# Kernel optimization log

Hardware: AMD Instinct MI355X
Metric: run time of the kernel (lower is better)

## Reference

```python
import jax, jax.numpy as jnp
import numpy as np
from functools import partial

STRIDE = 32
NUM_CLASSES = 20
CONF_THRESH = 0.01
NMS_THRESH = 0.5
H = W = 96
C = 512


def setup_inputs() -> dict:
    key = jax.random.key(0)
    ks = jax.random.split(key, 6)
    cls_feat = jax.random.normal(ks[0], (1, C, H, W), dtype=jnp.float32)
    reg_feat = jax.random.normal(ks[1], (1, C, H, W), dtype=jnp.float32)
    # small init scale so sigmoid/exp stay in a realistic range
    obj_w = jax.random.normal(ks[2], (1, C), dtype=jnp.float32) * 0.05
    cls_w = jax.random.normal(ks[3], (NUM_CLASSES, C), dtype=jnp.float32) * 0.05
    reg_w = jax.random.normal(ks[4], (4, C), dtype=jnp.float32) * 0.05
    obj_b = jnp.zeros((1,), jnp.float32)
    cls_b = jnp.zeros((NUM_CLASSES,), jnp.float32)
    reg_b = jnp.zeros((4,), jnp.float32)
    return {"cls_feat": cls_feat, "reg_feat": reg_feat,
            "obj_w": obj_w, "obj_b": obj_b,
            "cls_w": cls_w, "cls_b": cls_b,
            "reg_w": reg_w, "reg_b": reg_b}


def _decode_and_score(cls_feat, reg_feat, obj_w, obj_b, cls_w, cls_b, reg_w, reg_b):
    # 1x1 convs == per-pixel matmul; permute(0,2,3,1).flatten(1,2), take batch 0
    _, _, h, w = cls_feat.shape
    obj = jnp.einsum('bchw,oc->bhwo', cls_feat, obj_w)[0].reshape(h * w, 1) + obj_b
    cls = jnp.einsum('bchw,oc->bhwo', cls_feat, cls_w)[0].reshape(h * w, NUM_CLASSES) + cls_b
    reg = jnp.einsum('bchw,oc->bhwo', reg_feat, reg_w)[0].reshape(h * w, 4) + reg_b
    scores_all = jax.nn.sigmoid(obj) * jax.nn.sigmoid(cls)            # [N, 20]
    # decode_boxes: grid of (x, y) cell coords, stride 32
    gy, gx = jnp.meshgrid(jnp.arange(h), jnp.arange(w), indexing='ij')
    grid = jnp.stack([gx, gy], axis=-1).reshape(-1, 2).astype(jnp.float32)
    ctr = (jax.nn.sigmoid(reg[:, :2]) + grid) * STRIDE               # [N, 2]
    wh = jnp.exp(reg[:, 2:]) * STRIDE                                # [N, 2]
    bboxes = jnp.concatenate([ctr - 0.5 * wh, ctr + 0.5 * wh], axis=-1)  # x1y1x2y2
    return bboxes, scores_all


@jax.jit
def reference(cls_feat, reg_feat, obj_w, obj_b, cls_w, cls_b, reg_w, reg_b):
    bboxes, scores_all = _decode_and_score(
        cls_feat, reg_feat, obj_w, obj_b, cls_w, cls_b, reg_w, reg_b)
    n = bboxes.shape[0]
    labels = jnp.argmax(scores_all, axis=1)                          # [N]
    scores = jnp.max(scores_all, axis=1)                             # [N]
    valid = scores >= CONF_THRESH
    # sort by score descending (invalid boxes pushed last)
    order = jnp.argsort(-jnp.where(valid, scores, -jnp.inf))
    b = bboxes[order]
    lab_s = labels[order]
    valid_s = valid[order]
    x1, y1, x2, y2 = b[:, 0], b[:, 1], b[:, 2], b[:, 3]
    areas = (x2 - x1) * (y2 - y1)
    # pairwise IoU, matching the numpy nms (1e-10 clamp on w/h)
    iw = jnp.maximum(1e-10, jnp.minimum(x2[:, None], x2[None, :]) - jnp.maximum(x1[:, None], x1[None, :]))
    ih = jnp.maximum(1e-10, jnp.minimum(y2[:, None], y2[None, :]) - jnp.maximum(y1[:, None], y1[None, :]))
    inter = iw * ih
    iou = inter / (areas[:, None] + areas[None, :] - inter)
    same_cls = lab_s[:, None] == lab_s[None, :]
    supp = (iou > NMS_THRESH) & same_cls                             # [N, N] suppression graph
    idx = jnp.arange(n)
    # greedy per-class NMS in score order: box i is kept iff no earlier
    # kept box of the same class has IoU > thresh with it
    def body(i, keep):
        suppressed = jnp.any(keep & supp[:, i] & (idx < i))
        return keep.at[i].set(valid_s[i] & ~suppressed)
    keep_s = jax.lax.fori_loop(0, n, body, jnp.zeros(n, dtype=bool))
    keep = jnp.zeros(n, dtype=bool).at[order].set(keep_s)            # unsort
    return bboxes, scores, labels, keep


if __name__ == '__main__':
    out = reference(**setup_inputs())
    print([o.shape for o in out], int(out[3].sum()))
```

## Files before the change

kernel.cpp:

```cpp
#include <hip/hip_runtime.h>

#define HW 9216
#define WIDTH 96
#define NCLS 20
#define NOUT 25
#define CAP 1024
#define NW 16

__global__ __launch_bounds__(256) void decode_kernel(
    const float* __restrict__ cls_feat, const float* __restrict__ reg_feat,
    const float* __restrict__ obj_w, const float* __restrict__ obj_b,
    const float* __restrict__ cls_w, const float* __restrict__ cls_b,
    const float* __restrict__ reg_w, const float* __restrict__ reg_b,
    float* __restrict__ out, unsigned* __restrict__ cnt,
    unsigned long long* __restrict__ keys)
{
    __shared__ float lds[512 * 28];
    const int tid = threadIdx.x;

    for (int i = tid; i < 25 * 512; i += 256) {
        int o = i >> 9, c = i & 511;
        float v;
        if (o == 0)        v = obj_w[c];
        else if (o < 21)   v = cls_w[(o - 1) * 512 + c];
        else               v = reg_w[(o - 21) * 512 + c];
        lds[c * 28 + o] = v;
    }
    __syncthreads();

    const int posL  = tid & 31;
    const int chunk = tid >> 5;
    const int p     = blockIdx.x * 32 + posL;
    const int cb    = chunk * 64;

    float acc[NOUT];
#pragma unroll
    for (int o = 0; o < NOUT; ++o) acc[o] = 0.f;

    const float* cf = cls_feat + cb * HW + p;
    const float* rf = reg_feat + cb * HW + p;

#pragma unroll 4
    for (int k = 0; k < 64; ++k) {
        float f = cf[k * HW];
        float g = rf[k * HW];
        const float4* w = (const float4*)(lds + (cb + k) * 28);
        float4 w0 = w[0], w1 = w[1], w2 = w[2], w3 = w[3], w4v = w[4], w5 = w[5], w6 = w[6];
        acc[0]  += f * w0.x;  acc[1]  += f * w0.y;  acc[2]  += f * w0.z;  acc[3]  += f * w0.w;
        acc[4]  += f * w1.x;  acc[5]  += f * w1.y;  acc[6]  += f * w1.z;  acc[7]  += f * w1.w;
        acc[8]  += f * w2.x;  acc[9]  += f * w2.y;  acc[10] += f * w2.z;  acc[11] += f * w2.w;
        acc[12] += f * w3.x;  acc[13] += f * w3.y;  acc[14] += f * w3.z;  acc[15] += f * w3.w;
        acc[16] += f * w4v.x; acc[17] += f * w4v.y; acc[18] += f * w4v.z; acc[19] += f * w4v.w;
        acc[20] += f * w5.x;
        acc[21] += g * w5.y;  acc[22] += g * w5.z;  acc[23] += g * w5.w;  acc[24] += g * w6.x;
    }

    __syncthreads();
    float* part = lds;
#pragma unroll
    for (int o = 0; o < NOUT; ++o) part[(chunk * 32 + posL) * NOUT + o] = acc[o];
    __syncthreads();

    float* dots = lds + 8 * 32 * NOUT;
    for (int t = tid; t < 32 * NOUT; t += 256) {
        int pos = t / NOUT, o = t - pos * NOUT;
        float s = 0.f;
#pragma unroll
        for (int c2 = 0; c2 < 8; ++c2) s += part[(c2 * 32 + pos) * NOUT + o];
        dots[t] = s;
    }
    __syncthreads();

    if (tid < 32) {
        const int pos = tid;
        const int pp  = blockIdx.x * 32 + pos;
        const float* d = dots + pos * NOUT;

        float obj  = d[0] + obj_b[0];
        float best = d[1] + cls_b[0];
        int   bk   = 0;
#pragma unroll
        for (int k = 1; k < NCLS; ++k) {
            float v = d[1 + k] + cls_b[k];
            if (v > best) { best = v; bk = k; }
        }
        float sobj  = 1.f / (1.f + expf(-obj));
        float scls  = 1.f / (1.f + expf(-best));
        float score = sobj * scls;

        float r0 = d[21] + reg_b[0], r1 = d[22] + reg_b[1];
        float r2 = d[23] + reg_b[2], r3 = d[24] + reg_b[3];
        float gx = (float)(pp % WIDTH), gy = (float)(pp / WIDTH);
        float cx = (1.f / (1.f + expf(-r0)) + gx) * 32.f;
        float cy = (1.f / (1.f + expf(-r1)) + gy) * 32.f;
        float bw = expf(r2) * 32.f;
        float bh = expf(r3) * 32.f;
        float hx = 0.5f * bw, hy = 0.5f * bh;

        ((float4*)out)[pp] = make_float4(cx - hx, cy - hy, cx + hx, cy + hy);
        out[HW * 4 + pp] = score;
        out[HW * 5 + pp] = (float)bk;
        out[HW * 6 + pp] = 0.f;

        if (score >= 0.01f) {
            unsigned slot = atomicAdd(&cnt[bk], 1u);
            if (slot < CAP) {
                unsigned sb = __float_as_uint(score) ^ 0xffffffffu;
                keys[bk * CAP + slot] = ((unsigned long long)sb << 32) | (unsigned)pp;
            }
        }
    }
}

__global__ __launch_bounds__(512) void sort_kernel(
    const unsigned* __restrict__ cnt, unsigned long long* __restrict__ keys)
{
    __shared__ unsigned long long a[CAP];
    const int c = blockIdx.x, t = threadIdx.x;
    unsigned m = cnt[c]; if (m > CAP) m = CAP;

    for (int i = t; i < CAP; i += 512)
        a[i] = (i < (int)m) ? keys[c * CAP + i] : 0xFFFFFFFFFFFFFFFFull;
    __syncthreads();

    for (int k = 2; k <= CAP; k <<= 1) {
        for (int j = k >> 1; j > 0; j >>= 1) {
            int i = ((t & ~(j - 1)) << 1) | (t & (j - 1));
            int p = i | j;
            unsigned long long x = a[i], y = a[p];
            bool up = ((i & k) == 0);
            if ((x > y) == up) { a[i] = y; a[p] = x; }
            __syncthreads();
        }
    }
    for (int i = t; i < (int)m; i += 512) keys[c * CAP + i] = a[i];
}

__global__ __launch_bounds__(1024) void build_kernel(
    const unsigned* __restrict__ cnt, const unsigned long long* __restrict__ keys,
    const float* __restrict__ bboxes, unsigned long long* __restrict__ mask)
{
    __shared__ float4 box[CAP];
    const int c = blockIdx.x >> 4, tile = blockIdx.x & 15;
    const int tid = threadIdx.x, wave = tid >> 6, lane = tid & 63;
    int m = (int)cnt[c]; if (m > CAP) m = CAP;
    const int rbase = tile << 6;
    if (rbase >= m) return;

    if (tid < m) {
        unsigned idx = (unsigned)(keys[c * CAP + tid] & 0xffffffffu);
        box[tid] = ((const float4*)bboxes)[idx];
    } else {
        box[tid] = make_float4(0.f, 0.f, 0.f, 0.f);
    }
    __syncthreads();

    unsigned long long* mrow = mask + (size_t)c * CAP * NW;
#pragma unroll 4
    for (int j = 0; j < 64; ++j) {
        const int row = rbase + (wave << 2) + (j >> 4);
        const int w   = j & 15;
        const float4 bi = box[row];
        const float4 bj = box[(w << 6) + lane];
        const float ai = (bi.z - bi.x) * (bi.w - bi.y);
        const float aj = (bj.z - bj.x) * (bj.w - bj.y);
        float iw = fminf(bi.z, bj.z) - fmaxf(bi.x, bj.x);
        float ih = fminf(bi.w, bj.w) - fmaxf(bi.y, bj.y);
        iw = fmaxf(iw, 1e-10f);
        ih = fmaxf(ih, 1e-10f);
        const float inter = iw * ih;
        const float iou = inter / (ai + aj - inter);
        unsigned long long word =
            __ballot((row < m) && (((w << 6) + lane) < m) && (iou > 0.5f));
        if (lane == 0) mrow[row * NW + w] = word;
    }
}

__device__ __forceinline__ unsigned long long uread64(unsigned long long v, int srclane) {
    unsigned lo = __builtin_amdgcn_readlane((unsigned)v, srclane);
    unsigned hi = __builtin_amdgcn_readlane((unsigned)(v >> 32), srclane);
    return ((unsigned long long)hi << 32) | lo;
}

__device__ __forceinline__ unsigned long long shflxor64(unsigned long long v, int m) {
    unsigned lo = __shfl_xor((unsigned)v, m, 64);
    unsigned hi = __shfl_xor((unsigned)(v >> 32), m, 64);
    return ((unsigned long long)hi << 32) | lo;
}

__global__ __launch_bounds__(64) void sweep_kernel(
    const unsigned* __restrict__ cnt, const unsigned long long* __restrict__ keys,
    const unsigned long long* __restrict__ mask, float* __restrict__ keep)
{
    const int c = blockIdx.x, lane = threadIdx.x;
    int m = (int)cnt[c]; if (m > CAP) m = CAP;
    const int nw = (m + 63) >> 6;
    const unsigned long long* mrow = mask + (size_t)c * CAP * NW;

    const int wsel = lane & 15;
    const int rof  = lane >> 4;

    unsigned long long remw = 0;
    for (int w = 0; w < nw; ++w) {
        const int i0 = w << 6;
        const int nb = min(64, m - i0);

        unsigned long long mykey =
            (lane < nb) ? keys[c * CAP + i0 + lane] : 0ull;
        unsigned long long myrow =
            (lane < nb) ? mrow[(size_t)(i0 + lane) * NW + w] : 0ull;

        unsigned long long rw[16];
#pragma unroll
        for (int j = 0; j < 16; ++j) {
            const int r = i0 + rof + (j << 2);
            rw[j] = (r < m && wsel < nw)
                        ? mrow[(size_t)r * NW + wsel] : 0ull;
        }

        unsigned long long cur  = uread64(remw, w);
        unsigned long long kept = 0;
#pragma unroll
        for (int b = 0; b < 64; ++b) {
            unsigned long long v = uread64(myrow, b);
            unsigned long long alive = ((cur >> b) & 1ull) ^ 1ull;
            kept |= alive << b;
            cur |= v & (0ull - alive);
        }
        if (nb < 64) kept &= (1ull << nb) - 1ull;

        if (lane < nb && ((kept >> lane) & 1ull))
            keep[(unsigned)(mykey & 0xffffffffu)] = 1.0f;

        unsigned long long part = 0;
#pragma unroll
        for (int j = 0; j < 16; ++j) {
            const int b = rof + (j << 2);
            part |= rw[j] & (0ull - ((kept >> b) & 1ull));
        }
        part |= shflxor64(part, 16);
        part |= shflxor64(part, 32);
        if (lane < NW) remw |= part;
    }
}

extern "C" void kernel_launch(void* const* d_in, const int* in_sizes, int n_in,
                              void* d_out, int out_size, void* d_ws, size_t ws_size,
                              hipStream_t stream)
{
    const float* cls_feat = (const float*)d_in[0];
    const float* reg_feat = (const float*)d_in[1];
    const float* obj_w    = (const float*)d_in[2];
    const float* obj_b    = (const float*)d_in[3];
    const float* cls_w    = (const float*)d_in[4];
    const float* cls_b    = (const float*)d_in[5];
    const float* reg_w    = (const float*)d_in[6];
    const float* reg_b    = (const float*)d_in[7];

    float* out = (float*)d_out;
    unsigned* cnt = (unsigned*)d_ws;
    unsigned long long* keys = (unsigned long long*)((char*)d_ws + 256);
    unsigned long long* mask = (unsigned long long*)((char*)d_ws + 256 + NCLS * CAP * 8);

    hipMemsetAsync(d_ws, 0, 256, stream);

    decode_kernel<<<288, 256, 0, stream>>>(cls_feat, reg_feat, obj_w, obj_b,
                                           cls_w, cls_b, reg_w, reg_b,
                                           out, cnt, keys);
    sort_kernel<<<NCLS, 512, 0, stream>>>(cnt, keys);
    build_kernel<<<NCLS * 16, 1024, 0, stream>>>(cnt, keys, out, mask);
    sweep_kernel<<<NCLS, 64, 0, stream>>>(cnt, keys, mask, out + HW * 6);
}
```

Measured before the change: 187.5 us.

## Split GEMM into channel-parallel stage, fuse sort, mask build and sweep into one kernel

The 1x1-conv GEMM now runs as a separate stage where each block handles 256 pixels for one 64-channel group, reading weights directly from global/scalar memory, and writes partial sums to workspace. A second kernel reduces the partials and decodes boxes. Sort, IoU mask construction and the greedy sweep are merged into a single per-class 1024-thread kernel that uses a register/shuffle bitonic sort and keeps the suppression mask in LDS. The memset is replaced by zeroing counters inside the first kernel. This removes launches and global mask traffic, at the cost of a partial-sum round trip and a serial per-class block with heavy LDS use.

```diff
diff --git a/kernel.cpp b/kernel.cpp
--- a/kernel.cpp
+++ b/kernel.cpp
@@ -7,240 +7,218 @@
 #define CAP 1024
 #define NW 16
 
-__global__ __launch_bounds__(256) void decode_kernel(
+#define WS_KEYS   256
+#define WS_PART   164096
+
+__global__ __launch_bounds__(256) void gemm_stage1(
     const float* __restrict__ cls_feat, const float* __restrict__ reg_feat,
-    const float* __restrict__ obj_w, const float* __restrict__ obj_b,
-    const float* __restrict__ cls_w, const float* __restrict__ cls_b,
-    const float* __restrict__ reg_w, const float* __restrict__ reg_b,
+    const float* __restrict__ obj_w, const float* __restrict__ cls_w,
+    const float* __restrict__ reg_w, float* __restrict__ partial,
+    unsigned* __restrict__ cnt)
+{
+    if (blockIdx.x == 0 && threadIdx.x < 64) cnt[threadIdx.x] = 0u;
+
+    const int g   = blockIdx.x & 7;
+    const int pos = (blockIdx.x >> 3) * 256 + threadIdx.x;
+    const int cb  = g * 64;
+
+    float acc[NOUT];
+#pragma unroll
+    for (int o = 0; o < NOUT; ++o) acc[o] = 0.f;
+
+    const float* cf = cls_feat + (size_t)cb * HW + pos;
+    const float* rf = reg_feat + (size_t)cb * HW + pos;
+
+#pragma unroll 16
+    for (int k = 0; k < 64; ++k) {
+        const int c = cb + k;
+        float f = cf[(size_t)k * HW];
+        float h = rf[(size_t)k * HW];
+        acc[0] += f * obj_w[c];
+#pragma unroll
+        for (int j = 0; j < 20; ++j) acc[1 + j] += f * cls_w[j * 512 + c];
+#pragma unroll
+        for (int j = 0; j < 4; ++j)  acc[21 + j] += h * reg_w[j * 512 + c];
+    }
+
+    float* pg = partial + (size_t)g * NOUT * HW + pos;
+#pragma unroll
+    for (int o = 0; o < NOUT; ++o) pg[(size_t)o * HW] = acc[o];
+}
+
+__global__ __launch_bounds__(256) void decode_stage2(
+    const float* __restrict__ partial,
+    const float* __restrict__ obj_b, const float* __restrict__ cls_b,
+    const float* __restrict__ reg_b,
     float* __restrict__ out, unsigned* __restrict__ cnt,
     unsigned long long* __restrict__ keys)
 {
-    __shared__ float lds[512 * 28];
-    const int tid = threadIdx.x;
-
-    for (int i = tid; i < 25 * 512; i += 256) {
-        int o = i >> 9, c = i & 511;
-        float v;
-        if (o == 0)        v = obj_w[c];
-        else if (o < 21)   v = cls_w[(o - 1) * 512 + c];
-        else               v = reg_w[(o - 21) * 512 + c];
-        lds[c * 28 + o] = v;
-    }
-    __syncthreads();
-
-    const int posL  = tid & 31;
-    const int chunk = tid >> 5;
-    const int p     = blockIdx.x * 32 + posL;
-    const int cb    = chunk * 64;
-
-    float acc[NOUT];
-#pragma unroll
-    for (int o = 0; o < NOUT; ++o) acc[o] = 0.f;
-
-    const float* cf = cls_feat + cb * HW + p;
-    const float* rf = reg_feat + cb * HW + p;
-
-#pragma unroll 4
-    for (int k = 0; k < 64; ++k) {
-        float f = cf[k * HW];
-        float g = rf[k * HW];
-        const float4* w = (const float4*)(lds + (cb + k) * 28);
-        float4 w0 = w[0], w1 = w[1], w2 = w[2], w3 = w[3], w4v = w[4], w5 = w[5], w6 = w[6];
-        acc[0]  += f * w0.x;  acc[1]  += f * w0.y;  acc[2]  += f * w0.z;  acc[3]  += f * w0.w;
-        acc[4]  += f * w1.x;  acc[5]  += f * w1.y;  acc[6]  += f * w1.z;  acc[7]  += f * w1.w;
-        acc[8]  += f * w2.x;  acc[9]  += f * w2.y;  acc[10] += f * w2.z;  acc[11] += f * w2.w;
-        acc[12] += f * w3.x;  acc[13] += f * w3.y;  acc[14] += f * w3.z;  acc[15] += f * w3.w;
-        acc[16] += f * w4v.x; acc[17] += f * w4v.y; acc[18] += f * w4v.z; acc[19] += f * w4v.w;
-        acc[20] += f * w5.x;
-        acc[21] += g * w5.y;  acc[22] += g * w5.z;  acc[23] += g * w5.w;  acc[24] += g * w6.x;
-    }
-
-    __syncthreads();
-    float* part = lds;
-#pragma unroll
-    for (int o = 0; o < NOUT; ++o) part[(chunk * 32 + posL) * NOUT + o] = acc[o];
-    __syncthreads();
-
-    float* dots = lds + 8 * 32 * NOUT;
-    for (int t = tid; t < 32 * NOUT; t += 256) {
-        int pos = t / NOUT, o = t - pos * NOUT;
+    const int pp = blockIdx.x * 256 + threadIdx.x;
+
+    float d[NOUT];
+#pragma unroll
+    for (int o = 0; o < NOUT; ++o) {
         float s = 0.f;
 #pragma unroll
-        for (int c2 = 0; c2 < 8; ++c2) s += part[(c2 * 32 + pos) * NOUT + o];
-        dots[t] = s;
-    }
-    __syncthreads();
-
-    if (tid < 32) {
-        const int pos = tid;
-        const int pp  = blockIdx.x * 32 + pos;
-        const float* d = dots + pos * NOUT;
-
-        float obj  = d[0] + obj_b[0];
-        float best = d[1] + cls_b[0];
-        int   bk   = 0;
-#pragma unroll
-        for (int k = 1; k < NCLS; ++k) {
-            float v = d[1 + k] + cls_b[k];
-            if (v > best) { best = v; bk = k; }
-        }
-        float sobj  = 1.f / (1.f + expf(-obj));
-        float scls  = 1.f / (1.f + expf(-best));
-        float score = sobj * scls;
-
-        float r0 = d[21] + reg_b[0], r1 = d[22] + reg_b[1];
-        float r2 = d[23] + reg_b[2], r3 = d[24] + reg_b[3];
-        float gx = (float)(pp % WIDTH), gy = (float)(pp / WIDTH);
-        float cx = (1.f / (1.f + expf(-r0)) + gx) * 32.f;
-        float cy = (1.f / (1.f + expf(-r1)) + gy) * 32.f;
-        float bw = expf(r2) * 32.f;
-        float bh = expf(r3) * 32.f;
-        float hx = 0.5f * bw, hy = 0.5f * bh;
-
-        ((float4*)out)[pp] = make_float4(cx - hx, cy - hy, cx + hx, cy + hy);
-        out[HW * 4 + pp] = score;
-        out[HW * 5 + pp] = (float)bk;
-        out[HW * 6 + pp] = 0.f;
-
-        if (score >= 0.01f) {
-            unsigned slot = atomicAdd(&cnt[bk], 1u);
-            if (slot < CAP) {
-                unsigned sb = __float_as_uint(score) ^ 0xffffffffu;
-                keys[bk * CAP + slot] = ((unsigned long long)sb << 32) | (unsigned)pp;
-            }
-        }
-    }
-}
-
-__global__ __launch_bounds__(512) void sort_kernel(
-    const unsigned* __restrict__ cnt, unsigned long long* __restrict__ keys)
-{
-    __shared__ unsigned long long a[CAP];
-    const int c = blockIdx.x, t = threadIdx.x;
-    unsigned m = cnt[c]; if (m > CAP) m = CAP;
-
-    for (int i = t; i < CAP; i += 512)
-        a[i] = (i < (int)m) ? keys[c * CAP + i] : 0xFFFFFFFFFFFFFFFFull;
-    __syncthreads();
-
-    for (int k = 2; k <= CAP; k <<= 1) {
-        for (int j = k >> 1; j > 0; j >>= 1) {
-            int i = ((t & ~(j - 1)) << 1) | (t & (j - 1));
-            int p = i | j;
-            unsigned long long x = a[i], y = a[p];
-            bool up = ((i & k) == 0);
-            if ((x > y) == up) { a[i] = y; a[p] = x; }
-            __syncthreads();
-        }
-    }
-    for (int i = t; i < (int)m; i += 512) keys[c * CAP + i] = a[i];
-}
-
-__global__ __launch_bounds__(1024) void build_kernel(
-    const unsigned* __restrict__ cnt, const unsigned long long* __restrict__ keys,
-    const float* __restrict__ bboxes, unsigned long long* __restrict__ mask)
-{
-    __shared__ float4 box[CAP];
-    const int c = blockIdx.x >> 4, tile = blockIdx.x & 15;
-    const int tid = threadIdx.x, wave = tid >> 6, lane = tid & 63;
-    int m = (int)cnt[c]; if (m > CAP) m = CAP;
-    const int rbase = tile << 6;
-    if (rbase >= m) return;
-
-    if (tid < m) {
-        unsigned idx = (unsigned)(keys[c * CAP + tid] & 0xffffffffu);
-        box[tid] = ((const float4*)bboxes)[idx];
-    } else {
-        box[tid] = make_float4(0.f, 0.f, 0.f, 0.f);
-    }
-    __syncthreads();
-
-    unsigned long long* mrow = mask + (size_t)c * CAP * NW;
-#pragma unroll 4
-    for (int j = 0; j < 64; ++j) {
-        const int row = rbase + (wave << 2) + (j >> 4);
-        const int w   = j & 15;
-        const float4 bi = box[row];
-        const float4 bj = box[(w << 6) + lane];
-        const float ai = (bi.z - bi.x) * (bi.w - bi.y);
-        const float aj = (bj.z - bj.x) * (bj.w - bj.y);
-        float iw = fminf(bi.z, bj.z) - fmaxf(bi.x, bj.x);
-        float ih = fminf(bi.w, bj.w) - fmaxf(bi.y, bj.y);
-        iw = fmaxf(iw, 1e-10f);
-        ih = fmaxf(ih, 1e-10f);
-        const float inter = iw * ih;
-        const float iou = inter / (ai + aj - inter);
-        unsigned long long word =
-            __ballot((row < m) && (((w << 6) + lane) < m) && (iou > 0.5f));
-        if (lane == 0) mrow[row * NW + w] = word;
-    }
-}
-
+        for (int g = 0; g < 8; ++g)
+            s += partial[((size_t)g * NOUT + o) * HW + pp];
+        d[o] = s;
+    }
+
+    float obj  = d[0] + obj_b[0];
+    float best = d[1] + cls_b[0];
+    int   bk   = 0;
+#pragma unroll
+    for (int k = 1; k < NCLS; ++k) {
+        float v = d[1 + k] + cls_b[k];
+        if (v > best) { best = v; bk = k; }
+    }
+    float sobj  = 1.f / (1.f + expf(-obj));
+    float scls  = 1.f / (1.f + expf(-best));
+    float score = sobj * scls;
+
+    float r0 = d[21] + reg_b[0], r1 = d[22] + reg_b[1];
+    float r2 = d[23] + reg_b[2], r3 = d[24] + reg_b[3];
+    float gx = (float)(pp % WIDTH), gy = (float)(pp / WIDTH);
+    float cx = (1.f / (1.f + expf(-r0)) + gx) * 32.f;
+    float cy = (1.f / (1.f + expf(-r1)) + gy) * 32.f;
+    float bw = expf(r2) * 32.f;
+    float bh = expf(r3) * 32.f;
+    float hx = 0.5f * bw, hy = 0.5f * bh;
+
+    ((float4*)out)[pp] = make_float4(cx - hx, cy - hy, cx + hx, cy + hy);
+    out[HW * 4 + pp] = score;
+    out[HW * 5 + pp] = (float)bk;
+    out[HW * 6 + pp] = 0.f;
+
+    if (score >= 0.01f) {
+        unsigned slot = atomicAdd(&cnt[bk], 1u);
+        if (slot < CAP) {
+            unsigned sb = __float_as_uint(score) ^ 0xffffffffu;
+            keys[bk * CAP + slot] = ((unsigned long long)sb << 32) | (unsigned)pp;
+        }
+    }
+}
+
+__device__ __forceinline__ unsigned long long shflxor64(unsigned long long v, int msk) {
+    unsigned lo = __shfl_xor((unsigned)v, msk, 64);
+    unsigned hi = __shfl_xor((unsigned)(v >> 32), msk, 64);
+    return ((unsigned long long)hi << 32) | lo;
+}
 __device__ __forceinline__ unsigned long long uread64(unsigned long long v, int srclane) {
     unsigned lo = __builtin_amdgcn_readlane((unsigned)v, srclane);
     unsigned hi = __builtin_amdgcn_readlane((unsigned)(v >> 32), srclane);
     return ((unsigned long long)hi << 32) | lo;
 }
 
-__device__ __forceinline__ unsigned long long shflxor64(unsigned long long v, int m) {
-    unsigned lo = __shfl_xor((unsigned)v, m, 64);
-    unsigned hi = __shfl_xor((unsigned)(v >> 32), m, 64);
-    return ((unsigned long long)hi << 32) | lo;
-}
-
-__global__ __launch_bounds__(64) void sweep_kernel(
+__global__ __launch_bounds__(1024) void nms_fused(
     const unsigned* __restrict__ cnt, const unsigned long long* __restrict__ keys,
-    const unsigned long long* __restrict__ mask, float* __restrict__ keep)
-{
-    const int c = blockIdx.x, lane = threadIdx.x;
+    const float* __restrict__ bboxes, float* __restrict__ keep)
+{
+    __shared__ unsigned long long smask[CAP * NW];
+    __shared__ float4  box[CAP];
+    __shared__ unsigned lidx[CAP];
+
+    const int c = blockIdx.x, tid = threadIdx.x;
+    const int wave = tid >> 6, lane = tid & 63;
     int m = (int)cnt[c]; if (m > CAP) m = CAP;
     const int nw = (m + 63) >> 6;
-    const unsigned long long* mrow = mask + (size_t)c * CAP * NW;
-
-    const int wsel = lane & 15;
-    const int rof  = lane >> 4;
-
-    unsigned long long remw = 0;
-    for (int w = 0; w < nw; ++w) {
-        const int i0 = w << 6;
-        const int nb = min(64, m - i0);
-
-        unsigned long long mykey =
-            (lane < nb) ? keys[c * CAP + i0 + lane] : 0ull;
-        unsigned long long myrow =
-            (lane < nb) ? mrow[(size_t)(i0 + lane) * NW + w] : 0ull;
-
-        unsigned long long rw[16];
-#pragma unroll
-        for (int j = 0; j < 16; ++j) {
-            const int r = i0 + rof + (j << 2);
-            rw[j] = (r < m && wsel < nw)
-                        ? mrow[(size_t)r * NW + wsel] : 0ull;
-        }
-
-        unsigned long long cur  = uread64(remw, w);
-        unsigned long long kept = 0;
-#pragma unroll
-        for (int b = 0; b < 64; ++b) {
-            unsigned long long v = uread64(myrow, b);
-            unsigned long long alive = ((cur >> b) & 1ull) ^ 1ull;
-            kept |= alive << b;
-            cur |= v & (0ull - alive);
-        }
-        if (nb < 64) kept &= (1ull << nb) - 1ull;
-
-        if (lane < nb && ((kept >> lane) & 1ull))
-            keep[(unsigned)(mykey & 0xffffffffu)] = 1.0f;
-
-        unsigned long long part = 0;
-#pragma unroll
-        for (int j = 0; j < 16; ++j) {
-            const int b = rof + (j << 2);
-            part |= rw[j] & (0ull - ((kept >> b) & 1ull));
-        }
-        part |= shflxor64(part, 16);
-        part |= shflxor64(part, 32);
-        if (lane < NW) remw |= part;
+
+    unsigned long long v = (tid < m) ? keys[c * CAP + tid] : 0xFFFFFFFFFFFFFFFFull;
+    for (int k = 2; k <= CAP; k <<= 1) {
+        for (int j = k >> 1; j > 0; j >>= 1) {
+            unsigned long long u;
+            if (j >= 64) {
+                __syncthreads();
+                smask[tid] = v;
+                __syncthreads();
+                u = smask[tid ^ j];
+            } else {
+                u = shflxor64(v, j);
+            }
+            const bool takeSmall = (((tid & k) == 0) == ((tid & j) == 0));
+            const bool less = v < u;
+            v = (takeSmall == less) ? v : u;
+        }
+    }
+    __syncthreads();
+
+    for (int i = tid; i < CAP * NW; i += 1024) smask[i] = 0ull;
+    if (tid < m) {
+        unsigned idx = (unsigned)(v & 0xffffffffu);
+        lidx[tid] = idx;
+        box[tid]  = ((const float4*)bboxes)[idx];
+    } else {
+        box[tid] = make_float4(0.f, 0.f, 0.f, 0.f);
+    }
+    __syncthreads();
+
+    float jx1[16], jy1[16], jx2[16], jy2[16], jar[16];
+#pragma unroll
+    for (int w = 0; w < 16; ++w) {
+        float4 b = box[(w << 6) + lane];
+        jx1[w] = b.x; jy1[w] = b.y; jx2[w] = b.z; jy2[w] = b.w;
+        jar[w] = (b.z - b.x) * (b.w - b.y);
+    }
+    for (int r = wave; r < m; r += 16) {
+        const float4 bi = box[r];
+        const float ai = (bi.z - bi.x) * (bi.w - bi.y);
+#pragma unroll
+        for (int w = 0; w < 16; ++w) {
+            if (w >= nw) break;
+            const int j = (w << 6) + lane;
+            float iw = fminf(bi.z, jx2[w]) - fmaxf(bi.x, jx1[w]);
+            float ih = fminf(bi.w, jy2[w]) - fmaxf(bi.y, jy1[w]);
+            iw = fmaxf(iw, 1e-10f);
+            ih = fmaxf(ih, 1e-10f);
+            const float inter = iw * ih;
+            const float iou = inter / (ai + jar[w] - inter);
+            unsigned long long word = __ballot((j < m) && (iou > 0.5f));
+            if (lane == 0) smask[r * NW + w] = word;
+        }
+    }
+    __syncthreads();
+
+    if (wave == 0) {
+        const int wsel = lane & 15;
+        const int rof  = lane >> 4;
+        unsigned long long remw = 0;
+        for (int w = 0; w < nw; ++w) {
+            const int i0 = w << 6;
+            const int nb = min(64, m - i0);
+
+            unsigned long long myrow =
+                (lane < nb) ? smask[(i0 + lane) * NW + w] : 0ull;
+
+            unsigned long long rw[16];
+#pragma unroll
+            for (int j = 0; j < 16; ++j)
+                rw[j] = smask[(i0 + rof + (j << 2)) * NW + wsel];
+
+            unsigned long long cur  = uread64(remw, w);
+            unsigned long long kept = 0;
+#pragma unroll
+            for (int b = 0; b < 64; ++b) {
+                unsigned long long x = uread64(myrow, b);
+                unsigned long long alive = ((cur >> b) & 1ull) ^ 1ull;
+                kept |= alive << b;
+                cur |= x & (0ull - alive);
+            }
+            if (nb < 64) kept &= (1ull << nb) - 1ull;
+
+            if (lane < nb && ((kept >> lane) & 1ull))
+                keep[lidx[i0 + lane]] = 1.0f;
+
+            unsigned long long part = 0;
+#pragma unroll
+            for (int j = 0; j < 16; ++j) {
+                const int b = rof + (j << 2);
+                part |= rw[j] & (0ull - ((kept >> b) & 1ull));
+            }
+            part |= shflxor64(part, 16);
+            part |= shflxor64(part, 32);
+            if (lane < NW) remw |= part;
+        }
     }
 }
 
@@ -258,16 +236,13 @@
     const float* reg_b    = (const float*)d_in[7];
 
     float* out = (float*)d_out;
-    unsigned* cnt = (unsigned*)d_ws;
-    unsigned long long* keys = (unsigned long long*)((char*)d_ws + 256);
-    unsigned long long* mask = (unsigned long long*)((char*)d_ws + 256 + NCLS * CAP * 8);
-
-    hipMemsetAsync(d_ws, 0, 256, stream);
-
-    decode_kernel<<<288, 256, 0, stream>>>(cls_feat, reg_feat, obj_w, obj_b,
-                                           cls_w, cls_b, reg_w, reg_b,
-                                           out, cnt, keys);
-    sort_kernel<<<NCLS, 512, 0, stream>>>(cnt, keys);
-    build_kernel<<<NCLS * 16, 1024, 0, stream>>>(cnt, keys, out, mask);
-    sweep_kernel<<<NCLS, 64, 0, stream>>>(cnt, keys, mask, out + HW * 6);
-}
+    unsigned* cnt            = (unsigned*)d_ws;
+    unsigned long long* keys = (unsigned long long*)((char*)d_ws + WS_KEYS);
+    float* partial           = (float*)((char*)d_ws + WS_PART);
+
+    gemm_stage1<<<288, 256, 0, stream>>>(cls_feat, reg_feat,
+                                         obj_w, cls_w, reg_w, partial, cnt);
+    decode_stage2<<<HW / 256, 256, 0, stream>>>(partial, obj_b, cls_b, reg_b,
+                                                out, cnt, keys);
+    nms_fused<<<NCLS, 1024, 0, stream>>>(cnt, keys, out, out + HW * 6);
+}
```

After: 269.3 us. 43.7% more time.
